# Performance work log

Hardware: AMD Instinct MI355X
Metric: run time of the kernel (lower is better)

## Reference

```python
import jax, jax.numpy as jnp
import numpy as np

NEG = -1000000000.0
EPS = 1e-05

def setup_inputs() -> dict:
    key = jax.random.key(0)
    k1, k2, k3, k4, k5 = jax.random.split(key, 5)
    B, L, E, Q = 64, 2048, 512, 256
    encoded_vecs = jax.random.normal(k1, (B, L, E), dtype=jnp.float32)
    query = jax.random.normal(k2, (B, Q), dtype=jnp.float32)
    length = jax.random.randint(k3, (B,), 1, L + 1, dtype=jnp.int32)
    # Xavier-normal-ish params
    W1 = jax.random.normal(k4, (E + Q, E), dtype=jnp.float32) * jnp.sqrt(2.0 / (E + Q + E))
    b1 = jnp.zeros((E,), dtype=jnp.float32)
    v = jax.random.normal(k5, (E,), dtype=jnp.float32) * jnp.sqrt(2.0 / (E + 1))
    return {"encoded_vecs": encoded_vecs, "query": query, "length": length,
            "W1": W1, "b1": b1, "v": v}

def reference(encoded_vecs, query, length, W1, b1, v):
    B, L, E = encoded_vecs.shape
    # broadcast 2D query over the length dim (repeat in torch code)
    q = jnp.broadcast_to(query[:, None, :], (B, L, query.shape[-1]))
    h = jnp.concatenate([encoded_vecs, q], axis=2)            # [B, L, E+Q]
    u = jnp.tanh(jnp.einsum('blc,ce->ble', h, W1) + b1)       # [B, L, E]
    logits = jnp.einsum('ble,e->bl', u, v)                    # [B, L]
    # masked softmax (faithful to masked_softmax in source)
    mask = (jnp.arange(L)[None, :] < length[:, None])         # [B, L] bool
    masked_logits = jnp.where(mask, logits, NEG)
    max_logits = jnp.max(masked_logits, axis=1, keepdims=True)
    exps = jnp.exp(masked_logits - max_logits) * mask.astype(logits.dtype)
    attention = exps / (jnp.sum(exps, axis=1, keepdims=True) + EPS)  # [B, L]
    context = jnp.einsum('bl,ble->be', attention, encoded_vecs)      # [B, E]
    return (context, attention)
```

## Files before the change

kernel.cpp:

```cpp
#include <hip/hip_runtime.h>

typedef __attribute__((ext_vector_type(4))) float float4v;
typedef __attribute__((ext_vector_type(2))) float float2v;
typedef __attribute__((ext_vector_type(8))) short short8;
typedef __attribute__((ext_vector_type(4))) float f32x4;
typedef __attribute__((ext_vector_type(4))) int int4v;

#define NEGV (-1000000000.0f)

#define MTOT (64 * 2048)

__device__ __forceinline__ unsigned short f2bf(float f) {
    unsigned int u = __float_as_uint(f);
    u += 0x7fffu + ((u >> 16) & 1u);
    return (unsigned short)(u >> 16);
}

__device__ __forceinline__ void gload_lds16(const void* g, void* l) {
    __builtin_amdgcn_global_load_lds(
        (__attribute__((address_space(1))) unsigned int*)(unsigned long long)(g),
        (__attribute__((address_space(3))) unsigned int*)(unsigned int)(unsigned long long)(l),
        16, 0, 0);
}

__global__ __launch_bounds__(256)
void prep_wt_kernel(const float* __restrict__ W1, unsigned short* __restrict__ Wt) {
    __shared__ float t[32][33];
    int bx = blockIdx.x & 15;
    int by = blockIdx.x >> 4;
    int tx = threadIdx.x & 31;
    int ty = threadIdx.x >> 5;
    #pragma unroll
    for (int i = 0; i < 4; ++i)
        t[ty + 8 * i][tx] = W1[(bx * 32 + ty + 8 * i) * 512 + by * 32 + tx];
    __syncthreads();
    #pragma unroll
    for (int i = 0; i < 4; ++i)
        Wt[(by * 32 + ty + 8 * i) * 512 + bx * 32 + tx] = f2bf(t[tx][ty + 8 * i]);
}

__global__ void prep_qc_kernel(const float* __restrict__ query, const float* __restrict__ W1,
                               const float* __restrict__ b1, float* __restrict__ qc) {
    int b = blockIdx.x;
    int e = threadIdx.x;
    float acc0 = b1[e];
    float acc1 = b1[e + 256];
    const float* w = W1 + 512 * 512;
    for (int q = 0; q < 256; ++q) {
        float qv = query[b * 256 + q];
        acc0 += qv * w[q * 512 + e];
        acc1 += qv * w[q * 512 + e + 256];
    }
    qc[b * 512 + e] = acc0;
    qc[b * 512 + e + 256] = acc1;
}

__global__ __launch_bounds__(256)
void gemm_logits_kernel(const float* __restrict__ A,
                        const unsigned short* __restrict__ Wt,
                        const float* __restrict__ qc,
                        const float* __restrict__ v,
                        const int* __restrict__ length,
                        float* __restrict__ part)
{
    int bid = blockIdx.x;
    int orig = (bid & 7) * 512 + (bid >> 3);
    int bm = orig >> 2;
    int bn = orig & 3;
    int b = bm >> 4;
    int l0 = (bm & 15) * 128;
    if (l0 >= length[b]) return;

    __shared__ float As[2][128 * 32];
    __shared__ unsigned short Bs[2][128 * 32];

    int tid = threadIdx.x;
    int lane = tid & 63;
    int w = tid >> 6;
    int wm = w >> 1, wn = w & 1;
    long row0 = (long)bm * 128;
    int col0 = bn * 128;

    const char* gA[4];
    const char* gB[2];
    #pragma unroll
    for (int i = 0; i < 4; ++i) {
        int off = (w * 4 + i) * 1024 + lane * 16;
        int r = off >> 7;
        int kbg = (off & 127) ^ ((r & 7) << 4);
        gA[i] = (const char*)A + (row0 + r) * 2048 + kbg;
    }
    #pragma unroll
    for (int i = 0; i < 2; ++i) {
        int off = (w * 2 + i) * 1024 + lane * 16;
        gB[i] = (const char*)Wt + (long)(col0 + (off >> 6)) * 1024 + (off & 63);
    }
    char* lA0 = (char*)&As[0][0] + w * 4096;
    char* lA1 = (char*)&As[1][0] + w * 4096;
    char* lB0 = (char*)&Bs[0][0] + w * 2048;
    char* lB1 = (char*)&Bs[1][0] + w * 2048;

    int aoff[4][2], boff[4];
    int kb0 = 32 * (lane >> 4);
    #pragma unroll
    for (int mi = 0; mi < 4; ++mi) {
        int ar = wm * 64 + (lane & 15) + mi * 16;
        int swz = (ar & 7) << 4;
        aoff[mi][0] = ar * 128 + (kb0 ^ swz);
        aoff[mi][1] = ar * 128 + ((kb0 + 16) ^ swz);
    }
    int kbB = 16 * (lane >> 4);
    #pragma unroll
    for (int ni = 0; ni < 4; ++ni)
        boff[ni] = (wn * 64 + (lane & 15) + ni * 16) * 64 + kbB;

    f32x4 acc[4][4] = {};

    auto STAGE = [&](int t, char* la, char* lb) {
        gload_lds16(gA[0] + t * 128, la);
        gload_lds16(gA[1] + t * 128, la + 1024);
        gload_lds16(gA[2] + t * 128, la + 2048);
        gload_lds16(gA[3] + t * 128, la + 3072);
        gload_lds16(gB[0] + t * 64, lb);
        gload_lds16(gB[1] + t * 64, lb + 1024);
    };
    auto COMPUTE = [&](const float* as, const unsigned short* bs) {
        short8 af[4], bf[4];
        #pragma unroll
        for (int mi = 0; mi < 4; ++mi) {
            float4v x = *(const float4v*)((const char*)as + aoff[mi][0]);
            float4v y = *(const float4v*)((const char*)as + aoff[mi][1]);
            union { int4v i; short8 s; } u;
            asm("v_cvt_pk_bf16_f32 %0, %1, %2" : "=v"(u.i.x) : "v"(x[0]), "v"(x[1]));
            asm("v_cvt_pk_bf16_f32 %0, %1, %2" : "=v"(u.i.y) : "v"(x[2]), "v"(x[3]));
            asm("v_cvt_pk_bf16_f32 %0, %1, %2" : "=v"(u.i.z) : "v"(y[0]), "v"(y[1]));
            asm("v_cvt_pk_bf16_f32 %0, %1, %2" : "=v"(u.i.w) : "v"(y[2]), "v"(y[3]));
            af[mi] = u.s;
        }
        #pragma unroll
        for (int ni = 0; ni < 4; ++ni)
            bf[ni] = *(const short8*)((const char*)bs + boff[ni]);
        #pragma unroll
        for (int mi = 0; mi < 4; ++mi)
            #pragma unroll
            for (int ni = 0; ni < 4; ++ni)
                acc[mi][ni] = __builtin_amdgcn_mfma_f32_16x16x32_bf16(af[mi], bf[ni], acc[mi][ni], 0, 0, 0);
    };

    STAGE(0, lA0, lB0);
    __syncthreads();
    #pragma unroll 1
    for (int ks = 0; ks < 16; ks += 2) {
        STAGE(ks + 1, lA1, lB1);
        COMPUTE(&As[0][0], &Bs[0][0]);
        __syncthreads();
        if (ks + 2 < 16) STAGE(ks + 2, lA0, lB0);
        COMPUTE(&As[1][0], &Bs[1][0]);
        __syncthreads();
    }

    const float* qcb = qc + b * 512;
    float vcol[4], qcol[4];
    #pragma unroll
    for (int ni = 0; ni < 4; ++ni) {
        int c = col0 + wn * 64 + ni * 16 + (lane & 15);
        vcol[ni] = v[c];
        qcol[ni] = qcb[c];
    }
    float* pslice = part + (bn * 2 + wn) * MTOT + row0;
    int rbase = wm * 64 + 4 * (lane >> 4);
    #pragma unroll
    for (int mi = 0; mi < 4; ++mi) {
        #pragma unroll
        for (int j = 0; j < 4; ++j) {
            float s = 0.f;
            #pragma unroll
            for (int ni = 0; ni < 4; ++ni) {
                float x = acc[mi][ni][j] + qcol[ni];
                float e2 = __expf(2.0f * x);
                float t = 1.0f - 2.0f * __builtin_amdgcn_rcpf(e2 + 1.0f);
                s += t * vcol[ni];
            }
            s += __shfl_xor(s, 1);
            s += __shfl_xor(s, 2);
            s += __shfl_xor(s, 4);
            s += __shfl_xor(s, 8);
            if ((lane & 15) == 0)
                pslice[rbase + mi * 16 + j] = s;
        }
    }
}

__global__ void softmax_kernel(const float* __restrict__ part, const int* __restrict__ length,
                               float* __restrict__ att, float* __restrict__ ctx) {
    int b = blockIdx.x;
    int len = length[b];
    int tid = threadIdx.x;
    int lane = tid & 63, wv = tid >> 6;
    const float* p0 = part + b * 2048;
    float* ab = att + b * 2048;

    ctx[b * 512 + tid] = 0.f;
    ctx[b * 512 + 256 + tid] = 0.f;

    float vals[8];
    float mymax = -3.402823466e38f;
    #pragma unroll
    for (int i = 0; i < 8; ++i) {
        int l = tid + i * 256;
        float x = NEGV;
        if (l < len) {
            x = 0.f;
            #pragma unroll
            for (int s = 0; s < 8; ++s)
                x += p0[s * MTOT + l];
        }
        vals[i] = x;
        mymax = fmaxf(mymax, x);
    }
    #pragma unroll
    for (int m = 32; m; m >>= 1) mymax = fmaxf(mymax, __shfl_xor(mymax, m));
    __shared__ float sm[4];
    if (lane == 0) sm[wv] = mymax;
    __syncthreads();
    float bmax = fmaxf(fmaxf(sm[0], sm[1]), fmaxf(sm[2], sm[3]));

    float mysum = 0.f;
    #pragma unroll
    for (int i = 0; i < 8; ++i) {
        int l = tid + i * 256;
        float e = (l < len) ? __expf(vals[i] - bmax) : 0.f;
        vals[i] = e;
        mysum += e;
    }
    #pragma unroll
    for (int m = 32; m; m >>= 1) mysum += __shfl_xor(mysum, m);
    __shared__ float ss[4];
    if (lane == 0) ss[wv] = mysum;
    __syncthreads();
    float tot = ss[0] + ss[1] + ss[2] + ss[3];
    float inv = 1.0f / (tot + 1e-5f);
    #pragma unroll
    for (int i = 0; i < 8; ++i) {
        int l = tid + i * 256;
        ab[l] = vals[i] * inv;
    }
}

__global__ void ctx_kernel(const float* __restrict__ att, const float* __restrict__ enc,
                           const int* __restrict__ length, float* __restrict__ ctx) {
    int b = blockIdx.x;
    int lc = blockIdx.y;
    int len = length[b];
    int l0 = lc * 128;
    if (l0 >= len) return;
    int lim = len - l0;
    if (lim > 128) lim = 128;

    int t = threadIdx.x;
    const float* ab = att + b * 2048 + l0;
    const float* eb = enc + ((long)(b * 2048 + l0)) * 512 + t * 2;
    float c0 = 0.f, c1 = 0.f;
    #pragma unroll 4
    for (int l = 0; l < lim; ++l) {
        float a = ab[l];
        float2v e = *(const float2v*)(eb);
        eb += 512;
        c0 += a * e.x;
        c1 += a * e.y;
    }
    atomicAdd(&ctx[b * 512 + 2 * t], c0);
    atomicAdd(&ctx[b * 512 + 2 * t + 1], c1);
}

extern "C" void kernel_launch(void* const* d_in, const int* in_sizes, int n_in,
                              void* d_out, int out_size, void* d_ws, size_t ws_size,
                              hipStream_t stream) {
    const float* enc    = (const float*)d_in[0];
    const float* query  = (const float*)d_in[1];
    const int*   length = (const int*)d_in[2];
    const float* W1     = (const float*)d_in[3];
    const float* b1     = (const float*)d_in[4];
    const float* v      = (const float*)d_in[5];

    float* out = (float*)d_out;
    float* ctx = out;
    float* att = out + 64 * 512;

    char* ws = (char*)d_ws;
    float* part        = (float*)ws;
    float* qc          = (float*)(ws + 8 * MTOT * 4);
    unsigned short* Wt = (unsigned short*)(ws + 8 * MTOT * 4 + 64 * 512 * 4);

    prep_wt_kernel<<<256, 256, 0, stream>>>(W1, Wt);
    prep_qc_kernel<<<64, 256, 0, stream>>>(query, W1, b1, qc);

    gemm_logits_kernel<<<4096, 256, 0, stream>>>(enc, Wt, qc, v, length, part);

    softmax_kernel<<<64, 256, 0, stream>>>(part, length, att, ctx);

    dim3 g3(64, 16);
    ctx_kernel<<<g3, 256, 0, stream>>>(att, enc, length, ctx);
}
```

Before: 146.1 us.

## Triple-buffer GEMM LDS pipeline with single barrier, swizzle B tiles, remap block order

Replaces the double-buffered K loop, which used two barriers per pair of stages, with a three-stage LDS ring. Each iteration does a partial vmcnt wait and one barrier while two tiles are in flight. The B tile in LDS gets an XOR swizzle to reduce bank conflicts on the bf16 fragment reads. The block-to-tile mapping changes so groups of 8 consecutive blocks share the same N column across adjacent M tiles, which should improve L2 reuse. The cost is 50% more LDS per block, which may lower occupancy.

After: 152.2 us. 1.04x slower.

```diff
diff --git a/kernel.cpp b/kernel.cpp
--- a/kernel.cpp
+++ b/kernel.cpp
@@ -64,15 +64,16 @@
                         float* __restrict__ part)
 {
     int bid = blockIdx.x;
-    int orig = (bid & 7) * 512 + (bid >> 3);
-    int bm = orig >> 2;
-    int bn = orig & 3;
+    int x = bid & 7;
+    int j = bid >> 3;
+    int bm = (j >> 2) * 8 + x;
+    int bn = j & 3;
     int b = bm >> 4;
     int l0 = (bm & 15) * 128;
     if (l0 >= length[b]) return;
 
-    __shared__ float As[2][128 * 32];
-    __shared__ unsigned short Bs[2][128 * 32];
+    __shared__ float As[3 * 128 * 32];
+    __shared__ unsigned short Bs[3 * 128 * 32];
 
     int tid = threadIdx.x;
     int lane = tid & 63;
@@ -93,12 +94,10 @@
     #pragma unroll
     for (int i = 0; i < 2; ++i) {
         int off = (w * 2 + i) * 1024 + lane * 16;
-        gB[i] = (const char*)Wt + (long)(col0 + (off >> 6)) * 1024 + (off & 63);
-    }
-    char* lA0 = (char*)&As[0][0] + w * 4096;
-    char* lA1 = (char*)&As[1][0] + w * 4096;
-    char* lB0 = (char*)&Bs[0][0] + w * 2048;
-    char* lB1 = (char*)&Bs[1][0] + w * 2048;
+        int r = off >> 6;
+        int kbg = (off & 63) ^ (((r >> 1) & 3) << 4);
+        gB[i] = (const char*)Wt + (long)(col0 + r) * 1024 + kbg;
+    }
 
     int aoff[4][2], boff[4];
     int kb0 = 32 * (lane >> 4);
@@ -111,35 +110,37 @@
     }
     int kbB = 16 * (lane >> 4);
     #pragma unroll
-    for (int ni = 0; ni < 4; ++ni)
-        boff[ni] = (wn * 64 + (lane & 15) + ni * 16) * 64 + kbB;
+    for (int ni = 0; ni < 4; ++ni) {
+        int br = wn * 64 + (lane & 15) + ni * 16;
+        boff[ni] = br * 64 + (kbB ^ (((br >> 1) & 3) << 4));
+    }
 
     f32x4 acc[4][4] = {};
 
     auto STAGE = [&](int t, char* la, char* lb) {
-        gload_lds16(gA[0] + t * 128, la);
-        gload_lds16(gA[1] + t * 128, la + 1024);
-        gload_lds16(gA[2] + t * 128, la + 2048);
-        gload_lds16(gA[3] + t * 128, la + 3072);
-        gload_lds16(gB[0] + t * 64, lb);
-        gload_lds16(gB[1] + t * 64, lb + 1024);
+        gload_lds16(gA[0] + t * 128, la + w * 4096);
+        gload_lds16(gA[1] + t * 128, la + w * 4096 + 1024);
+        gload_lds16(gA[2] + t * 128, la + w * 4096 + 2048);
+        gload_lds16(gA[3] + t * 128, la + w * 4096 + 3072);
+        gload_lds16(gB[0] + t * 64, lb + w * 2048);
+        gload_lds16(gB[1] + t * 64, lb + w * 2048 + 1024);
     };
-    auto COMPUTE = [&](const float* as, const unsigned short* bs) {
+    auto COMPUTE = [&](const char* as, const char* bs) {
         short8 af[4], bf[4];
         #pragma unroll
         for (int mi = 0; mi < 4; ++mi) {
-            float4v x = *(const float4v*)((const char*)as + aoff[mi][0]);
-            float4v y = *(const float4v*)((const char*)as + aoff[mi][1]);
+            float4v xv = *(const float4v*)(as + aoff[mi][0]);
+            float4v yv = *(const float4v*)(as + aoff[mi][1]);
             union { int4v i; short8 s; } u;
-            asm("v_cvt_pk_bf16_f32 %0, %1, %2" : "=v"(u.i.x) : "v"(x[0]), "v"(x[1]));
-            asm("v_cvt_pk_bf16_f32 %0, %1, %2" : "=v"(u.i.y) : "v"(x[2]), "v"(x[3]));
-            asm("v_cvt_pk_bf16_f32 %0, %1, %2" : "=v"(u.i.z) : "v"(y[0]), "v"(y[1]));
-            asm("v_cvt_pk_bf16_f32 %0, %1, %2" : "=v"(u.i.w) : "v"(y[2]), "v"(y[3]));
+            asm("v_cvt_pk_bf16_f32 %0, %1, %2" : "=v"(u.i.x) : "v"(xv[0]), "v"(xv[1]));
+            asm("v_cvt_pk_bf16_f32 %0, %1, %2" : "=v"(u.i.y) : "v"(xv[2]), "v"(xv[3]));
+            asm("v_cvt_pk_bf16_f32 %0, %1, %2" : "=v"(u.i.z) : "v"(yv[0]), "v"(yv[1]));
+            asm("v_cvt_pk_bf16_f32 %0, %1, %2" : "=v"(u.i.w) : "v"(yv[2]), "v"(yv[3]));
             af[mi] = u.s;
         }
         #pragma unroll
         for (int ni = 0; ni < 4; ++ni)
-            bf[ni] = *(const short8*)((const char*)bs + boff[ni]);
+            bf[ni] = *(const short8*)(bs + boff[ni]);
         #pragma unroll
         for (int mi = 0; mi < 4; ++mi)
             #pragma unroll
@@ -147,17 +148,29 @@
                 acc[mi][ni] = __builtin_amdgcn_mfma_f32_16x16x32_bf16(af[mi], bf[ni], acc[mi][ni], 0, 0, 0);
     };
 
-    STAGE(0, lA0, lB0);
-    __syncthreads();
+    char* Ab = (char*)As;
+    char* Bb = (char*)Bs;
+
+    STAGE(0, Ab, Bb);
+    STAGE(1, Ab + 16384, Bb + 8192);
+
+    int cur = 0;
     #pragma unroll 1
-    for (int ks = 0; ks < 16; ks += 2) {
-        STAGE(ks + 1, lA1, lB1);
-        COMPUTE(&As[0][0], &Bs[0][0]);
-        __syncthreads();
-        if (ks + 2 < 16) STAGE(ks + 2, lA0, lB0);
-        COMPUTE(&As[1][0], &Bs[1][0]);
-        __syncthreads();
-    }
+    for (int t = 0; t < 15; ++t) {
+        asm volatile("s_waitcnt vmcnt(6)" ::: "memory");
+        __builtin_amdgcn_s_barrier();
+        asm volatile("" ::: "memory");
+        if (t < 14) {
+            int tgt = cur == 0 ? 2 : cur - 1;
+            STAGE(t + 2, Ab + tgt * 16384, Bb + tgt * 8192);
+        }
+        COMPUTE(Ab + cur * 16384, Bb + cur * 8192);
+        cur = cur == 2 ? 0 : cur + 1;
+    }
+    asm volatile("s_waitcnt vmcnt(0)" ::: "memory");
+    __builtin_amdgcn_s_barrier();
+    asm volatile("" ::: "memory");
+    COMPUTE(Ab + cur * 16384, Bb + cur * 8192);
 
     const float* qcb = qc + b * 512;
     float vcol[4], qcol[4];
@@ -172,21 +185,21 @@
     #pragma unroll
     for (int mi = 0; mi < 4; ++mi) {
         #pragma unroll
-        for (int j = 0; j < 4; ++j) {
+        for (int j2 = 0; j2 < 4; ++j2) {
             float s = 0.f;
             #pragma unroll
             for (int ni = 0; ni < 4; ++ni) {
-                float x = acc[mi][ni][j] + qcol[ni];
-                float e2 = __expf(2.0f * x);
-                float t = 1.0f - 2.0f * __builtin_amdgcn_rcpf(e2 + 1.0f);
-                s += t * vcol[ni];
+                float xx = acc[mi][ni][j2] + qcol[ni];
+                float e2 = __expf(2.0f * xx);
+                float tt = 1.0f - 2.0f * __builtin_amdgcn_rcpf(e2 + 1.0f);
+                s += tt * vcol[ni];
             }
             s += __shfl_xor(s, 1);
             s += __shfl_xor(s, 2);
             s += __shfl_xor(s, 4);
             s += __shfl_xor(s, 8);
             if ((lane & 15) == 0)
-                pslice[rbase + mi * 16 + j] = s;
+                pslice[rbase + mi * 16 + j2] = s;
         }
     }
 }
@@ -208,15 +221,15 @@
     #pragma unroll
     for (int i = 0; i < 8; ++i) {
         int l = tid + i * 256;
-        float x = NEGV;
+        float xv = NEGV;
         if (l < len) {
-            x = 0.f;
+            xv = 0.f;
             #pragma unroll
             for (int s = 0; s < 8; ++s)
-                x += p0[s * MTOT + l];
+                xv += p0[s * MTOT + l];
         }
-        vals[i] = x;
-        mymax = fmaxf(mymax, x);
+        vals[i] = xv;
+        mymax = fmaxf(mymax, xv);
     }
     #pragma unroll
     for (int m = 32; m; m >>= 1) mymax = fmaxf(mymax, __shfl_xor(mymax, m));
```
